# Performance work log

Measured on AMD Instinct MI355X. Metric: run time of the kernel, lower is better.

Reference implementation:

```python
import jax, jax.numpy as jnp
import numpy as np

H = 12  # num_attention_heads

def setup_inputs() -> dict:
    key = jax.random.key(0)
    ks = jax.random.split(key, 6)
    B, S, D = 2, 2048, 768
    sc = 0.02
    return {
        "hidden_states": jax.random.normal(ks[0], (B, S, D), jnp.float32),
        "Wqr": jax.random.normal(ks[1], (D, D), jnp.float32) * sc,
        "Wqi": jax.random.normal(ks[2], (D, D), jnp.float32) * sc,
        "Wkr": jax.random.normal(ks[3], (D, D), jnp.float32) * sc,
        "Wki": jax.random.normal(ks[4], (D, D), jnp.float32) * sc,
        "Wv": jax.random.normal(ks[5], (D, D), jnp.float32) * sc,
    }

def _heads(x, B, S):
    # [B,S,D] -> [B,H,S,Dh]
    return x.reshape(B, S, H, -1).transpose(0, 2, 1, 3)

def reference(hidden_states, Wqr, Wqi, Wkr, Wki, Wv):
    B, S, D = hidden_states.shape
    Dh = D // H
    x = hidden_states  # real input; imag part is zero
    # complex projections with zero imag input: q = (x@Wqr.T) + i (x@Wqi.T), same for k
    qr = _heads(x @ Wqr.T, B, S)
    qi = _heads(x @ Wqi.T, B, S)
    kr = _heads(x @ Wkr.T, B, S)
    ki = _heads(x @ Wki.T, B, S)
    v = _heads(x @ Wv.T, B, S)
    scale = 1.0 / jnp.sqrt(jnp.float32(Dh))
    # complex QK^H in real arithmetic: s = q @ conj(k)^T
    sr = (jnp.einsum('bhqd,bhkd->bhqk', qr, kr) +
          jnp.einsum('bhqd,bhkd->bhqk', qi, ki)) * scale
    si = (jnp.einsum('bhqd,bhkd->bhqk', qi, kr) -
          jnp.einsum('bhqd,bhkd->bhqk', qr, ki)) * scale
    scores = jnp.sqrt(sr * sr + si * si)  # 'magnitude' variant
    probs = jax.nn.softmax(scores, axis=-1)
    ctx = jnp.einsum('bhqk,bhkd->bhqd', probs, v)
    return ctx.transpose(0, 2, 1, 3).reshape(B, S, D)
```

## Files before the change

kernel.cpp:

```cpp
#include <hip/hip_runtime.h>
#include <cstdint>

typedef short bf16x8 __attribute__((ext_vector_type(8)));
typedef float f32x4 __attribute__((ext_vector_type(4)));

#define MFMA16(a, b, c) __builtin_amdgcn_mfma_f32_16x16x32_bf16((a), (b), (c), 0, 0, 0)

__device__ __forceinline__ void gl16(const unsigned short* g, unsigned short* l) {
  __builtin_amdgcn_global_load_lds(
      (const __attribute__((address_space(1))) unsigned int*)g,
      (__attribute__((address_space(3))) unsigned int*)l, 16, 0, 0);
}

__device__ __forceinline__ unsigned short f2b(float f) {
  union { float f; unsigned int u; } x; x.f = f;
  unsigned int r = x.u + 0x7fffu + ((x.u >> 16) & 1u);
  return (unsigned short)(r >> 16);
}

__device__ __forceinline__ unsigned int pack2(float lo, float hi) {
  union { float f; unsigned int u; } a, b;
  a.f = lo; b.f = hi;
  return ((a.u + 0x8000u) >> 16) | ((b.u + 0x8000u) & 0xffff0000u);
}

#define NB 2
#define NS 2048
#define ND 768
#define NH 12
#define DHD 64
#define MTOK 4096

#define OFF_XB 0
#define OFF_WB 3145728
#define OFF_QK 6094848
#define OFF_VT 18677760

__global__ void cvt_kernel(const float* __restrict__ src,
                           unsigned short* __restrict__ dst, int n4, float scale) {
  int i = blockIdx.x * blockDim.x + threadIdx.x;
  if (i >= n4) return;
  float4 v = ((const float4*)src)[i];
  ushort4 o;
  o.x = f2b(v.x * scale); o.y = f2b(v.y * scale);
  o.z = f2b(v.z * scale); o.w = f2b(v.w * scale);
  ((ushort4*)dst)[i] = o;
}

__global__ void wcvt_kernel(const float* __restrict__ s0, const float* __restrict__ s1,
                            const float* __restrict__ s2, const float* __restrict__ s3,
                            const float* __restrict__ s4, unsigned short* __restrict__ dst,
                            float qs) {
  const int bz = blockIdx.x / 576;
  const int i = (blockIdx.x % 576) * 256 + threadIdx.x;
  const float* src = bz == 0 ? s0 : bz == 1 ? s1 : bz == 2 ? s2 : bz == 3 ? s3 : s4;
  const float scale = bz < 2 ? qs : 1.0f;
  float4 v = ((const float4*)src)[i];
  ushort4 o;
  o.x = f2b(v.x * scale); o.y = f2b(v.y * scale);
  o.z = f2b(v.z * scale); o.w = f2b(v.w * scale);
  ((ushort4*)(dst + bz * 589824))[i] = o;
}

__global__ __launch_bounds__(512) void proj_kernel(
    const unsigned short* __restrict__ Xb, const unsigned short* __restrict__ Wb,
    unsigned short* __restrict__ QK, unsigned short* __restrict__ Vt) {
  __shared__ __align__(16) unsigned short S[65536];

  const int lin = blockIdx.x;
  const int sb = (lin & 7) * 30 + (lin >> 3);
  const int z = sb / 48;
  const int rem = sb % 48;
  const int m0 = (rem / 3) * 256;
  const int n0 = (rem % 3) * 256;

  const unsigned short* Wz = Wb + z * 589824;
  const int tid = threadIdx.x;
  const int lane = tid & 63;
  const int w = tid >> 6;
  const int wm = (w >> 2) * 128;
  const int wn = (w & 3) * 64;
  const int col = lane & 15, quad = lane >> 4;
  const int c7 = col & 7;

  const int lr = lane >> 3;
  const int lc = (lane & 7) ^ (lr & 7);
  const unsigned short* gX = Xb + (m0 + w * 8 + lr) * ND + lc * 8;
  const unsigned short* gW = Wz + (n0 + w * 8 + lr) * ND + lc * 8;
  const int stg = (w * 8) * 64;

  f32x4 acc[8][4] = {};

#pragma unroll
  for (int i = 0; i < 4; i++) {
    gl16(gX + i * (64 * ND), S + stg + i * 4096);
    gl16(gW + i * (64 * ND), S + 32768 + stg + i * 4096);
  }
  __syncthreads();

  int cur = 0;
  for (int kk = 0; kk < 12; kk++) {
    if (kk < 11) {
      const int k0n = (kk + 1) * 64;
      unsigned short* dA = S + ((cur ^ 1) * 16384) + stg;
      unsigned short* dB = S + 32768 + ((cur ^ 1) * 16384) + stg;
#pragma unroll
      for (int i = 0; i < 4; i++) {
        gl16(gX + i * (64 * ND) + k0n, dA + i * 4096);
        gl16(gW + i * (64 * ND) + k0n, dB + i * 4096);
      }
    }
    const unsigned short* Ac = S + cur * 16384;
    const unsigned short* Bc = S + 32768 + cur * 16384;
#pragma unroll
    for (int ks = 0; ks < 2; ks++) {
      const int fo = (((ks * 4 + quad) ^ c7) * 8);
      bf16x8 af[8], bw[4];
#pragma unroll
      for (int t = 0; t < 8; t++)
        af[t] = *(const bf16x8*)(Ac + (wm + t * 16 + col) * 64 + fo);
#pragma unroll
      for (int u = 0; u < 4; u++)
        bw[u] = *(const bf16x8*)(Bc + (wn + u * 16 + col) * 64 + fo);
#pragma unroll
      for (int mt = 0; mt < 8; mt++)
#pragma unroll
        for (int nt = 0; nt < 4; nt++)
          acc[mt][nt] = MFMA16(af[mt], bw[nt], acc[mt][nt]);
    }
    __syncthreads();
    cur ^= 1;
  }

  unsigned short* T = S;

  if (z < 4) {
    unsigned short* out = QK + z * (MTOK * ND);
    const int wrow = w >> 2;
#pragma unroll
    for (int half = 0; half < 2; half++) {
      __syncthreads();
      if (wrow == half) {
#pragma unroll
        for (int mt = 0; mt < 8; mt++) {
          int rl = mt * 16 + quad * 4;
#pragma unroll
          for (int nt = 0; nt < 4; nt++) {
            int cl = wn + nt * 16 + col;
#pragma unroll
            for (int r = 0; r < 4; r++) T[(rl + r) * 264 + cl] = f2b(acc[mt][nt][r]);
          }
        }
      }
      __syncthreads();
#pragma unroll
      for (int p = 0; p < 8; p++) {
        int ci = p * 512 + tid;
        int row = ci >> 5;
        int c8 = (ci & 31) * 8;
        uint4 v = *(const uint4*)(T + row * 264 + c8);
        *(uint4*)(out + (m0 + half * 128 + row) * ND + n0 + c8) = v;
      }
    }
  } else {
    const int b = m0 >> 11;
    const int s_base = m0 & 2047;
    const int wcolh = (w & 3) >> 1;
#pragma unroll
    for (int half = 0; half < 2; half++) {
      __syncthreads();
      if (wcolh == half) {
        int clb = wn - half * 128;
#pragma unroll
        for (int mt = 0; mt < 8; mt++) {
          int rl = wm + mt * 16 + quad * 4;
#pragma unroll
          for (int nt = 0; nt < 4; nt++) {
            int cl = clb + nt * 16 + col;
            ushort4 pk;
            pk.x = f2b(acc[mt][nt][0]);
            pk.y = f2b(acc[mt][nt][1]);
            pk.z = f2b(acc[mt][nt][2]);
            pk.w = f2b(acc[mt][nt][3]);
            *(ushort4*)(T + cl * 264 + rl) = pk;
          }
        }
      }
      __syncthreads();
#pragma unroll
      for (int p = 0; p < 8; p++) {
        int ci = p * 512 + tid;
        int dhl = ci >> 5;
        int s8 = (ci & 31) * 8;
        int c = n0 + half * 128 + dhl;
        int h = c >> 6, dh = c & 63;
        uint4 v = *(const uint4*)(T + dhl * 264 + s8);
        *(uint4*)(Vt + ((b * NH + h) * DHD + dh) * NS + s_base + s8) = v;
      }
    }
  }
}

__global__ __launch_bounds__(256) void attn_kernel(
    const unsigned short* __restrict__ QK, const unsigned short* __restrict__ Vt,
    float* __restrict__ outp) {
  __shared__ __align__(16) unsigned short Krs[4096];
  __shared__ __align__(16) unsigned short Kis[4096];
  __shared__ __align__(16) unsigned short Vts[8192];
  __shared__ __align__(16) unsigned short Ps[4096];

  const int lin = blockIdx.x + 32 * (blockIdx.y + 12 * blockIdx.z);
  const int sb = (lin & 7) * 96 + (lin >> 3);
  const int qt = sb & 31;
  const int h = (sb >> 5) % 12;
  const int b = sb / 384;
  const int tid = threadIdx.x, lane = tid & 63, w = tid >> 6;
  const int col = lane & 15, quad = lane >> 4;
  const int c7 = col & 7;
  const int jb = quad ^ c7;
  const int f0 = jb * 8, f1 = (jb ^ 4) * 8;

  const unsigned short* Qr = QK;
  const unsigned short* Qi = QK + MTOK * ND;
  const unsigned short* Krp = QK + 2 * MTOK * ND;
  const unsigned short* Kip = QK + 3 * MTOK * ND;

  const int q_tok = b * NS + qt * 64 + w * 16 + col;
  const int qoff = q_tok * ND + h * DHD;

  bf16x8 qrf[2], qif[2], qrn[2];
#pragma unroll
  for (int kk = 0; kk < 2; kk++) {
    qrf[kk] = *(const bf16x8*)(Qr + qoff + kk * 32 + quad * 8);
    qif[kk] = *(const bf16x8*)(Qi + qoff + kk * 32 + quad * 8);
    qrn[kk] = qrf[kk] ^ (short)0x8000;
  }

  const int lr = lane >> 3;
  const int lc = (lane & 7) ^ (lr & 7);
  const unsigned short* gKr = Krp + (b * NS + w * 8 + lr) * ND + h * DHD + lc * 8;
  const unsigned short* gKi = Kip + (b * NS + w * 8 + lr) * ND + h * DHD + lc * 8;
  const unsigned short* gV = Vt + (b * NH + h) * (DHD * NS) + (w * 8 + lr) * NS + lc * 8;
  const int st = (w * 8) * 64;

  unsigned short* PsW = Ps + w * 1024;

  f32x4 o[4] = {};
  float lrow = 0.f;

  gl16(gKr, Krs + st);
  gl16(gKr + 32 * ND, Krs + st + 2048);
  gl16(gKi, Kis + st);
  gl16(gKi + 32 * ND, Kis + st + 2048);
  gl16(gV, Vts + st);
  gl16(gV + 32 * NS, Vts + st + 2048);
  gKr += 64 * ND;
  gKi += 64 * ND;
  gV += 64;

  int vb = 0;
  for (int kt = 0; kt < 32; kt++) {
    __syncthreads();

#pragma unroll
    for (int mt = 0; mt < 4; mt++) {
      f32x4 sr = {}, si = {};
      const int rowb = (mt * 16 + col) * 64;
      bf16x8 kr0 = *(const bf16x8*)(Krs + rowb + f0);
      bf16x8 ki0 = *(const bf16x8*)(Kis + rowb + f0);
      bf16x8 kr1 = *(const bf16x8*)(Krs + rowb + f1);
      bf16x8 ki1 = *(const bf16x8*)(Kis + rowb + f1);
      sr = MFMA16(kr0, qrf[0], sr);
      sr = MFMA16(ki0, qif[0], sr);
      si = MFMA16(kr0, qif[0], si);
      si = MFMA16(ki0, qrn[0], si);
      sr = MFMA16(kr1, qrf[1], sr);
      sr = MFMA16(ki1, qif[1], sr);
      si = MFMA16(kr1, qif[1], si);
      si = MFMA16(ki1, qrn[1], si);

      float e0, e1, e2, e3;
      {
        float m0f = __builtin_amdgcn_sqrtf(sr[0] * sr[0] + si[0] * si[0]);
        float m1f = __builtin_amdgcn_sqrtf(sr[1] * sr[1] + si[1] * si[1]);
        float m2f = __builtin_amdgcn_sqrtf(sr[2] * sr[2] + si[2] * si[2]);
        float m3f = __builtin_amdgcn_sqrtf(sr[3] * sr[3] + si[3] * si[3]);
        e0 = __builtin_amdgcn_exp2f(m0f);
        e1 = __builtin_amdgcn_exp2f(m1f);
        e2 = __builtin_amdgcn_exp2f(m2f);
        e3 = __builtin_amdgcn_exp2f(m3f);
      }
      lrow += (e0 + e1) + (e2 + e3);
      uint2 pk;
      pk.x = pack2(e0, e1);
      pk.y = pack2(e2, e3);
      *(uint2*)(PsW + col * 64 + (((mt * 2 + (quad >> 1)) ^ c7) * 8) + (quad & 1) * 4) = pk;
    }

    __syncthreads();

    if (kt < 31) {
      const int nb = (vb ^ 1) * 4096;
      gl16(gKr, Krs + st);
      gl16(gKr + 32 * ND, Krs + st + 2048);
      gl16(gKi, Kis + st);
      gl16(gKi + 32 * ND, Kis + st + 2048);
      gl16(gV, Vts + nb + st);
      gl16(gV + 32 * NS, Vts + nb + st + 2048);
      gKr += 64 * ND;
      gKi += 64 * ND;
      gV += 64;
    }

    const unsigned short* Vc = Vts + vb * 4096;
    bf16x8 pb0 = *(const bf16x8*)(PsW + col * 64 + f0);
    bf16x8 pb1 = *(const bf16x8*)(PsW + col * 64 + f1);
#pragma unroll
    for (int dt = 0; dt < 4; dt++) {
      const int rowv = (dt * 16 + col) * 64;
      bf16x8 va0 = *(const bf16x8*)(Vc + rowv + f0);
      bf16x8 va1 = *(const bf16x8*)(Vc + rowv + f1);
      o[dt] = MFMA16(va0, pb0, o[dt]);
      o[dt] = MFMA16(va1, pb1, o[dt]);
    }
    vb ^= 1;
  }

  lrow += __shfl_xor(lrow, 16);
  lrow += __shfl_xor(lrow, 32);
  float inv_l = 1.0f / lrow;
  float* op = outp + (size_t)q_tok * ND + h * DHD;
#pragma unroll
  for (int dt = 0; dt < 4; dt++) {
    float4 v;
    v.x = o[dt][0] * inv_l;
    v.y = o[dt][1] * inv_l;
    v.z = o[dt][2] * inv_l;
    v.w = o[dt][3] * inv_l;
    *(float4*)(op + dt * 16 + quad * 4) = v;
  }
}

extern "C" void kernel_launch(void* const* d_in, const int* in_sizes, int n_in,
                              void* d_out, int out_size, void* d_ws, size_t ws_size,
                              hipStream_t stream) {
  const float* X = (const float*)d_in[0];
  unsigned short* ws = (unsigned short*)d_ws;
  unsigned short* Xb = ws + OFF_XB;
  unsigned short* Wb = ws + OFF_WB;
  unsigned short* QK = ws + OFF_QK;
  unsigned short* Vt = ws + OFF_VT;

  const float QSCALE = 0.125f * 1.44269504088896f;

  cvt_kernel<<<3072, 256, 0, stream>>>(X, Xb, 786432, 1.0f);
  wcvt_kernel<<<2880, 256, 0, stream>>>((const float*)d_in[1], (const float*)d_in[2],
                                        (const float*)d_in[3], (const float*)d_in[4],
                                        (const float*)d_in[5], Wb, QSCALE);

  proj_kernel<<<240, 512, 0, stream>>>(Xb, Wb, QK, Vt);
  attn_kernel<<<dim3(32, 12, 2), 256, 0, stream>>>(QK, Vt, (float*)d_out);
}
```

Measured before the change: 183.5 us.

## Prefetch two K-tiles ahead with partial vmcnt waits in projection GEMM

Restructures the projection GEMM main loop so two K-tiles are in flight. Each iteration waits only for the older batch of global-to-LDS loads (vmcnt(8)) instead of draining everything with __syncthreads, then issues the next loads into the buffer it just consumed. The last tile is peeled out of the loop. This aims to hide global load latency behind the MFMA work, at the cost of relying on exact vmcnt accounting and an extra barrier per iteration.

After: 187.8 us. 1.02x slower.

```diff
diff --git a/kernel.cpp b/kernel.cpp
--- a/kernel.cpp
+++ b/kernel.cpp
@@ -96,22 +96,58 @@
     gl16(gX + i * (64 * ND), S + stg + i * 4096);
     gl16(gW + i * (64 * ND), S + 32768 + stg + i * 4096);
   }
-  __syncthreads();
-
-  int cur = 0;
-  for (int kk = 0; kk < 12; kk++) {
-    if (kk < 11) {
-      const int k0n = (kk + 1) * 64;
-      unsigned short* dA = S + ((cur ^ 1) * 16384) + stg;
-      unsigned short* dB = S + 32768 + ((cur ^ 1) * 16384) + stg;
+#pragma unroll
+  for (int i = 0; i < 4; i++) {
+    gl16(gX + i * (64 * ND) + 64, S + 16384 + stg + i * 4096);
+    gl16(gW + i * (64 * ND) + 64, S + 49152 + stg + i * 4096);
+  }
+
+  for (int kk = 0; kk < 11; kk++) {
+    asm volatile("s_waitcnt vmcnt(8)" ::: "memory");
+    __builtin_amdgcn_s_barrier();
+    asm volatile("" ::: "memory");
+
+    const unsigned short* Ac = S + (kk & 1) * 16384;
+    const unsigned short* Bc = S + 32768 + (kk & 1) * 16384;
+#pragma unroll
+    for (int ks = 0; ks < 2; ks++) {
+      const int fo = (((ks * 4 + quad) ^ c7) * 8);
+      bf16x8 af[8], bw[4];
+#pragma unroll
+      for (int t = 0; t < 8; t++)
+        af[t] = *(const bf16x8*)(Ac + (wm + t * 16 + col) * 64 + fo);
+#pragma unroll
+      for (int u = 0; u < 4; u++)
+        bw[u] = *(const bf16x8*)(Bc + (wn + u * 16 + col) * 64 + fo);
+#pragma unroll
+      for (int mt = 0; mt < 8; mt++)
+#pragma unroll
+        for (int nt = 0; nt < 4; nt++)
+          acc[mt][nt] = MFMA16(af[mt], bw[nt], acc[mt][nt]);
+    }
+
+    asm volatile("" ::: "memory");
+    __builtin_amdgcn_s_barrier();
+    asm volatile("" ::: "memory");
+
+    if (kk < 10) {
+      const int k0n = (kk + 2) * 64;
+      unsigned short* dA = S + (kk & 1) * 16384 + stg;
+      unsigned short* dB = S + 32768 + (kk & 1) * 16384 + stg;
 #pragma unroll
       for (int i = 0; i < 4; i++) {
         gl16(gX + i * (64 * ND) + k0n, dA + i * 4096);
         gl16(gW + i * (64 * ND) + k0n, dB + i * 4096);
       }
     }
-    const unsigned short* Ac = S + cur * 16384;
-    const unsigned short* Bc = S + 32768 + cur * 16384;
+  }
+
+  asm volatile("s_waitcnt vmcnt(0)" ::: "memory");
+  __builtin_amdgcn_s_barrier();
+  asm volatile("" ::: "memory");
+  {
+    const unsigned short* Ac = S + 16384;
+    const unsigned short* Bc = S + 49152;
 #pragma unroll
     for (int ks = 0; ks < 2; ks++) {
       const int fo = (((ks * 4 + quad) ^ c7) * 8);
@@ -128,8 +164,6 @@
         for (int nt = 0; nt < 4; nt++)
           acc[mt][nt] = MFMA16(af[mt], bw[nt], acc[mt][nt]);
     }
-    __syncthreads();
-    cur ^= 1;
   }
 
   unsigned short* T = S;
```
